# Optimization experiments

Measured on AMD Instinct MI355X. Metric: run time of the kernel, lower is better.

## Reference

```python
import jax, jax.numpy as jnp
import numpy as np

N_TOKEN = 16384
N_EMBED = 512


def setup_inputs() -> dict:
    key = jax.random.key(0)
    k1, k2, k3, k4 = jax.random.split(key, 4)
    inputs = jax.random.normal(k1, (8, 2048, N_EMBED), dtype=jnp.float32)
    # nn.Linear(n_embed, n_token): weight [n_token, n_embed], bias [n_token]
    lin_w = jax.random.normal(k2, (N_TOKEN, N_EMBED), dtype=jnp.float32) * (1.0 / np.sqrt(N_EMBED))
    lin_b = jax.random.normal(k3, (N_TOKEN,), dtype=jnp.float32) * 0.01
    # nn.Embedding(n_token, n_embed) weight = value embeddings
    value_w = jax.random.normal(k4, (N_TOKEN, N_EMBED), dtype=jnp.float32)
    return {"inputs": inputs, "lin_w": lin_w, "lin_b": lin_b, "value_w": value_w}


def reference(inputs, lin_w, lin_b, value_w):
    size = inputs.shape
    x = inputs.reshape(-1, N_EMBED)                       # [T, E]
    logits = jnp.einsum('te,ne->tn', x, lin_w) + lin_b    # [T, N]
    probs = jax.nn.softmax(logits, axis=-1)               # [T, N]
    quantized = jnp.einsum('tn,ne->te', probs, value_w) + x
    return quantized.reshape(size)
```

## Files before the change

### kernel.cpp

```cpp
#include <hip/hip_runtime.h>
#include <hip/hip_bf16.h>
#include <stdint.h>

#define N_TOKEN 16384
#define N_EMBED 512
#define QBLK 64
#define KVB 64
#define NT (N_TOKEN / KVB)

typedef __attribute__((ext_vector_type(8))) short bf16x8;
typedef __attribute__((ext_vector_type(4))) float f32x4;

__device__ __forceinline__ unsigned short f2bf(float f) {
  unsigned u = __float_as_uint(f);
  u = (u + 0x7FFFu + ((u >> 16) & 1u)) >> 16;
  return (unsigned short)u;
}
__device__ __forceinline__ float bf2f(unsigned short h) {
  return __uint_as_float(((unsigned)h) << 16);
}

__device__ __forceinline__ void load_lds16(const void* g, void* l) {
  __builtin_amdgcn_global_load_lds((const __attribute__((address_space(1))) void*)g,
                                   (__attribute__((address_space(3))) void*)l, 16, 0, 0);
}

__global__ void cvt_bf16_kernel(const float* __restrict__ in, unsigned short* __restrict__ out, int n8) {
  int i = blockIdx.x * blockDim.x + threadIdx.x;
  if (i >= n8) return;
  float4 a = ((const float4*)in)[i * 2 + 0];
  float4 b = ((const float4*)in)[i * 2 + 1];
  uint4 o;
  o.x = (unsigned)f2bf(a.x) | ((unsigned)f2bf(a.y) << 16);
  o.y = (unsigned)f2bf(a.z) | ((unsigned)f2bf(a.w) << 16);
  o.z = (unsigned)f2bf(b.x) | ((unsigned)f2bf(b.y) << 16);
  o.w = (unsigned)f2bf(b.z) | ((unsigned)f2bf(b.w) << 16);
  ((uint4*)out)[i] = o;
}

__global__ void transpose_cvt_kernel(const float* __restrict__ in, unsigned short* __restrict__ out) {
  __shared__ float tile[64][65];
  int n0 = blockIdx.x * 64;
  int e0 = blockIdx.y * 64;
  int c = threadIdx.x & 63;
  int r0 = threadIdx.x >> 6;
#pragma unroll
  for (int r = r0; r < 64; r += 4)
    tile[r][c] = in[(size_t)(n0 + r) * N_EMBED + e0 + c];
  __syncthreads();
#pragma unroll
  for (int r = r0; r < 64; r += 4)
    out[(size_t)(e0 + r) * N_TOKEN + n0 + c] = f2bf(tile[c][r]);
}

__global__ __launch_bounds__(512, 2) void flash3_kernel(
    const unsigned short* __restrict__ xb,
    const unsigned short* __restrict__ kb,
    const unsigned short* __restrict__ vt,
    const float* __restrict__ bias,
    const float* __restrict__ xf,
    float* __restrict__ out)
{
  __shared__ __align__(16) unsigned char lds[131072 + 16384 + 8192 + 256];
  unsigned char* Ks = lds;
  unsigned char* Sp = lds + 131072;
  unsigned char* Pb = lds + 131072 + 16384;
  float* lsumB = (float*)(lds + 131072 + 16384 + 8192);

  const int tid = threadIdx.x;
  const int w = tid >> 6;
  const int lane = tid & 63;
  const int g = lane >> 4;
  const int l15 = lane & 15;
  const int wr = w >> 1, we = w & 1;
  const int qbase = blockIdx.x * QBLK;

  if (tid < 64) lsumB[tid] = 0.f;

  bf16x8 q[8];
#pragma unroll
  for (int kk = 0; kk < 8; ++kk)
    q[kk] = *(const bf16x8*)(xb + (size_t)(qbase + 16 * wr + l15) * N_EMBED + 256 * we + 32 * kk + 8 * g);

  const f32x4 fzero = {0.f, 0.f, 0.f, 0.f};
  f32x4 acc[4][4];
#pragma unroll
  for (int rf = 0; rf < 4; ++rf)
#pragma unroll
    for (int cf = 0; cf < 4; ++cf) acc[rf][cf] = fzero;

  auto stage = [&](int half, int t) {
    const unsigned char* kg = (const unsigned char*)(kb + (size_t)t * KVB * N_EMBED);
    unsigned char* Kd = Ks + half * 65536;
#pragma unroll
    for (int it = 0; it < 8; ++it) {
      int c = tid + 512 * it;
      int row = c >> 6;
      int cb = (c & 63) * 16;
      load_lds16(kg + row * 1024 + (cb ^ ((row & 7) << 4)), Kd + c * 16);
    }
  };

  stage(0, 0);

  for (int kt = 0; kt < NT; ++kt) {
    const int buf = kt & 1;
    const unsigned char* Kb = Ks + buf * 65536;

    bf16x8 bv[4][2];
    {
      const unsigned short* vbase = vt + kt * KVB + 8 * g;
#pragma unroll
      for (int cf = 0; cf < 4; ++cf)
#pragma unroll
        for (int ks = 0; ks < 2; ++ks)
          bv[cf][ks] = *(const bf16x8*)(vbase + (size_t)(64 * w + 16 * cf + l15) * N_TOKEN + 32 * ks);
    }

    if (kt + 1 < NT) {
      stage(buf ^ 1, kt + 1);
      asm volatile("s_waitcnt vmcnt(16)" ::: "memory");
    } else {
      asm volatile("s_waitcnt vmcnt(8)" ::: "memory");
    }
    __builtin_amdgcn_sched_barrier(0);
    __builtin_amdgcn_s_barrier();

    f32x4 s[4];
#pragma unroll
    for (int nf = 0; nf < 4; ++nf) s[nf] = fzero;
    __builtin_amdgcn_s_setprio(1);
#pragma unroll
    for (int kk = 0; kk < 8; ++kk) {
      int cb = 512 * we + 64 * kk + 16 * g;
#pragma unroll
      for (int nf = 0; nf < 4; ++nf) {
        int row = 16 * nf + l15;
        bf16x8 bk = *(const bf16x8*)(Kb + row * 1024 + (cb ^ ((row & 7) << 4)));
        s[nf] = __builtin_amdgcn_mfma_f32_16x16x32_bf16(q[kk], bk, s[nf], 0, 0, 0);
      }
    }
    __builtin_amdgcn_s_setprio(0);
#pragma unroll
    for (int nf = 0; nf < 4; ++nf)
#pragma unroll
      for (int j = 0; j < 4; ++j) {
        int row = 16 * wr + 4 * g + j;
        int slot = (2 * nf + (l15 >> 3)) ^ (row & 7);
        *(unsigned short*)(Sp + we * 8192 + row * 128 + 16 * slot + 2 * (l15 & 7)) = f2bf(s[nf][j]);
      }
    asm volatile("s_waitcnt lgkmcnt(0)" ::: "memory");
    __builtin_amdgcn_sched_barrier(0);
    __builtin_amdgcn_s_barrier();

    {
      int row = 8 * w + (lane >> 3);
      int c = lane & 7;
      int off = row * 128 + 16 * (c ^ (row & 7));
      bf16x8 p0 = *(const bf16x8*)(Sp + off);
      bf16x8 p1 = *(const bf16x8*)(Sp + 8192 + off);
      const float* bp = bias + kt * KVB + 8 * c;
      float4 b0 = *(const float4*)bp;
      float4 b1 = *(const float4*)(bp + 4);
      float bb[8] = {b0.x, b0.y, b0.z, b0.w, b1.x, b1.y, b1.z, b1.w};
      bf16x8 pw;
      float ps = 0.f;
#pragma unroll
      for (int i = 0; i < 8; ++i) {
        float v = exp2f((bf2f((unsigned short)p0[i]) + bf2f((unsigned short)p1[i]) + bb[i]) * 1.44269504f);
        pw[i] = (short)f2bf(v);
        ps += v;
      }
      *(bf16x8*)(Pb + off) = pw;
      ps += __shfl_xor(ps, 1, 64);
      ps += __shfl_xor(ps, 2, 64);
      ps += __shfl_xor(ps, 4, 64);
      if (c == 0) lsumB[row] += ps;
    }
    asm volatile("s_waitcnt lgkmcnt(0)" ::: "memory");
    __builtin_amdgcn_sched_barrier(0);
    __builtin_amdgcn_s_barrier();

    __builtin_amdgcn_s_setprio(1);
#pragma unroll
    for (int ks = 0; ks < 2; ++ks) {
      bf16x8 pa[4];
#pragma unroll
      for (int rf = 0; rf < 4; ++rf) {
        int row = 16 * rf + l15;
        pa[rf] = *(const bf16x8*)(Pb + row * 128 + 16 * ((4 * ks + g) ^ (row & 7)));
      }
#pragma unroll
      for (int cf = 0; cf < 4; ++cf)
#pragma unroll
        for (int rf = 0; rf < 4; ++rf)
          acc[rf][cf] = __builtin_amdgcn_mfma_f32_16x16x32_bf16(pa[rf], bv[cf][ks], acc[rf][cf], 0, 0, 0);
    }
    __builtin_amdgcn_s_setprio(0);
  }

#pragma unroll
  for (int rf = 0; rf < 4; ++rf)
#pragma unroll
    for (int j = 0; j < 4; ++j) {
      int lrow = 16 * rf + 4 * g + j;
      float inv = 1.0f / lsumB[lrow];
      int row = qbase + lrow;
#pragma unroll
      for (int cf = 0; cf < 4; ++cf) {
        int col = 64 * w + 16 * cf + l15;
        size_t idx = (size_t)row * N_EMBED + col;
        out[idx] = acc[rf][cf][j] * inv + xf[idx];
      }
    }
}

extern "C" void kernel_launch(void* const* d_in, const int* in_sizes, int n_in,
                              void* d_out, int out_size, void* d_ws, size_t ws_size,
                              hipStream_t stream) {
  const float* x = (const float*)d_in[0];
  const float* lin_w = (const float*)d_in[1];
  const float* lin_b = (const float*)d_in[2];
  const float* value_w = (const float*)d_in[3];
  float* outp = (float*)d_out;

  unsigned short* xb = (unsigned short*)d_ws;
  unsigned short* wb = (unsigned short*)((char*)d_ws + (16 << 20));
  unsigned short* vt = (unsigned short*)((char*)d_ws + (32 << 20));

  const int n8 = (N_TOKEN * N_EMBED) / 8;
  cvt_bf16_kernel<<<n8 / 256, 256, 0, stream>>>(x, xb, n8);
  cvt_bf16_kernel<<<n8 / 256, 256, 0, stream>>>(lin_w, wb, n8);
  transpose_cvt_kernel<<<dim3(N_TOKEN / 64, N_EMBED / 64), 256, 0, stream>>>(value_w, vt);
  flash3_kernel<<<N_TOKEN / QBLK, 512, 0, stream>>>(xb, wb, vt, lin_b, x, outp);
}
```

Measured before the change: 1.216 ms.

## Software-pipeline flash kernel over three stages with smaller key blocks

Halves the key/value block to 32 tokens and reorganises the main loop into a three-stage software pipeline: QK^T for tile t, softmax/exp for tile t-1 and PV accumulation for tile t-2 run in the same iteration, so each step needs one barrier instead of three. Waves are re-split so each computes all 64 query rows over a quarter of the embedding, and partial logits are reduced through double-buffered LDS. Row sums now stay in registers and are reduced once at the end. LDS use drops, but launch bounds go from 2 to 1 block per CU and q fragments take more registers, which may cut occupancy and latency hiding.

```diff
diff --git a/kernel.cpp b/kernel.cpp
--- a/kernel.cpp
+++ b/kernel.cpp
@@ -5,10 +5,11 @@
 #define N_TOKEN 16384
 #define N_EMBED 512
 #define QBLK 64
-#define KVB 64
+#define KVB 32
 #define NT (N_TOKEN / KVB)
 
 typedef __attribute__((ext_vector_type(8))) short bf16x8;
+typedef __attribute__((ext_vector_type(4))) short bf16x4;
 typedef __attribute__((ext_vector_type(4))) float f32x4;
 
 __device__ __forceinline__ unsigned short f2bf(float f) {
@@ -53,7 +54,7 @@
     out[(size_t)(e0 + r) * N_TOKEN + n0 + c] = f2bf(tile[c][r]);
 }
 
-__global__ __launch_bounds__(512, 2) void flash3_kernel(
+__global__ __launch_bounds__(512, 1) void flash4_kernel(
     const unsigned short* __restrict__ xb,
     const unsigned short* __restrict__ kb,
     const unsigned short* __restrict__ vt,
@@ -61,26 +62,27 @@
     const float* __restrict__ xf,
     float* __restrict__ out)
 {
-  __shared__ __align__(16) unsigned char lds[131072 + 16384 + 8192 + 256];
+  __shared__ __align__(16) unsigned char lds[65536 + 36864 + 8192 + 256];
   unsigned char* Ks = lds;
-  unsigned char* Sp = lds + 131072;
-  unsigned char* Pb = lds + 131072 + 16384;
-  float* lsumB = (float*)(lds + 131072 + 16384 + 8192);
+  unsigned char* Sp = lds + 65536;
+  unsigned char* Pb = lds + 65536 + 36864;
+  float* lsumB = (float*)(lds + 65536 + 36864 + 8192);
 
   const int tid = threadIdx.x;
   const int w = tid >> 6;
   const int lane = tid & 63;
   const int g = lane >> 4;
   const int l15 = lane & 15;
-  const int wr = w >> 1, we = w & 1;
+  const int we = w >> 1, wn = w & 1;
   const int qbase = blockIdx.x * QBLK;
 
-  if (tid < 64) lsumB[tid] = 0.f;
-
-  bf16x8 q[8];
-#pragma unroll
-  for (int kk = 0; kk < 8; ++kk)
-    q[kk] = *(const bf16x8*)(xb + (size_t)(qbase + 16 * wr + l15) * N_EMBED + 256 * we + 32 * kk + 8 * g);
+  bf16x8 q[4][4];
+#pragma unroll
+  for (int rf = 0; rf < 4; ++rf)
+#pragma unroll
+    for (int kk = 0; kk < 4; ++kk)
+      q[rf][kk] = *(const bf16x8*)(xb + (size_t)(qbase + 16 * rf + l15) * N_EMBED +
+                                   128 * we + 32 * kk + 8 * g);
 
   const f32x4 fzero = {0.f, 0.f, 0.f, 0.f};
   f32x4 acc[4][4];
@@ -88,12 +90,16 @@
   for (int rf = 0; rf < 4; ++rf)
 #pragma unroll
     for (int cf = 0; cf < 4; ++cf) acc[rf][cf] = fzero;
+  float lsum_reg = 0.f;
+
+  const int eq = 8 * w + (lane >> 3);
+  const int ec = lane & 7;
 
   auto stage = [&](int half, int t) {
     const unsigned char* kg = (const unsigned char*)(kb + (size_t)t * KVB * N_EMBED);
-    unsigned char* Kd = Ks + half * 65536;
-#pragma unroll
-    for (int it = 0; it < 8; ++it) {
+    unsigned char* Kd = Ks + half * 32768;
+#pragma unroll
+    for (int it = 0; it < 4; ++it) {
       int c = tid + 512 * it;
       int row = c >> 6;
       int cb = (c & 63) * 16;
@@ -103,109 +109,106 @@
 
   stage(0, 0);
 
-  for (int kt = 0; kt < NT; ++kt) {
-    const int buf = kt & 1;
-    const unsigned char* Kb = Ks + buf * 65536;
-
-    bf16x8 bv[4][2];
-    {
-      const unsigned short* vbase = vt + kt * KVB + 8 * g;
-#pragma unroll
-      for (int cf = 0; cf < 4; ++cf)
-#pragma unroll
-        for (int ks = 0; ks < 2; ++ks)
-          bv[cf][ks] = *(const bf16x8*)(vbase + (size_t)(64 * w + 16 * cf + l15) * N_TOKEN + 32 * ks);
-    }
-
-    if (kt + 1 < NT) {
-      stage(buf ^ 1, kt + 1);
-      asm volatile("s_waitcnt vmcnt(16)" ::: "memory");
-    } else {
-      asm volatile("s_waitcnt vmcnt(8)" ::: "memory");
-    }
+  for (int t = 0; t < NT + 2; ++t) {
+    asm volatile("s_waitcnt vmcnt(0) lgkmcnt(0)" ::: "memory");
     __builtin_amdgcn_sched_barrier(0);
     __builtin_amdgcn_s_barrier();
 
-    f32x4 s[4];
-#pragma unroll
-    for (int nf = 0; nf < 4; ++nf) s[nf] = fzero;
-    __builtin_amdgcn_s_setprio(1);
-#pragma unroll
-    for (int kk = 0; kk < 8; ++kk) {
-      int cb = 512 * we + 64 * kk + 16 * g;
-#pragma unroll
-      for (int nf = 0; nf < 4; ++nf) {
-        int row = 16 * nf + l15;
-        bf16x8 bk = *(const bf16x8*)(Kb + row * 1024 + (cb ^ ((row & 7) << 4)));
-        s[nf] = __builtin_amdgcn_mfma_f32_16x16x32_bf16(q[kk], bk, s[nf], 0, 0, 0);
+    bf16x8 bv[4];
+    if (t >= 2) {
+      const unsigned short* vbase = vt + (size_t)(t - 2) * KVB + 8 * g;
+#pragma unroll
+      for (int cf = 0; cf < 4; ++cf)
+        bv[cf] = *(const bf16x8*)(vbase + (size_t)(64 * w + 16 * cf + l15) * N_TOKEN);
+    }
+    if (t + 1 < NT) stage((t + 1) & 1, t + 1);
+
+    if (t < NT) {
+      const unsigned char* Kb = Ks + (t & 1) * 32768;
+      f32x4 s[4];
+#pragma unroll
+      for (int rf = 0; rf < 4; ++rf) s[rf] = fzero;
+      const int krow = 16 * wn + l15;
+      __builtin_amdgcn_s_setprio(1);
+#pragma unroll
+      for (int kk = 0; kk < 4; ++kk) {
+        int cb = 256 * we + 64 * kk + 16 * g;
+        bf16x8 bk = *(const bf16x8*)(Kb + krow * 1024 + (cb ^ ((krow & 7) << 4)));
+#pragma unroll
+        for (int rf = 0; rf < 4; ++rf)
+          s[rf] = __builtin_amdgcn_mfma_f32_16x16x32_bf16(q[rf][kk], bk, s[rf], 0, 0, 0);
       }
-    }
-    __builtin_amdgcn_s_setprio(0);
-#pragma unroll
-    for (int nf = 0; nf < 4; ++nf)
-#pragma unroll
-      for (int j = 0; j < 4; ++j) {
-        int row = 16 * wr + 4 * g + j;
-        int slot = (2 * nf + (l15 >> 3)) ^ (row & 7);
-        *(unsigned short*)(Sp + we * 8192 + row * 128 + 16 * slot + 2 * (l15 & 7)) = f2bf(s[nf][j]);
-      }
-    asm volatile("s_waitcnt lgkmcnt(0)" ::: "memory");
-    __builtin_amdgcn_sched_barrier(0);
-    __builtin_amdgcn_s_barrier();
-
-    {
-      int row = 8 * w + (lane >> 3);
-      int c = lane & 7;
-      int off = row * 128 + 16 * (c ^ (row & 7));
-      bf16x8 p0 = *(const bf16x8*)(Sp + off);
-      bf16x8 p1 = *(const bf16x8*)(Sp + 8192 + off);
-      const float* bp = bias + kt * KVB + 8 * c;
-      float4 b0 = *(const float4*)bp;
-      float4 b1 = *(const float4*)(bp + 4);
-      float bb[8] = {b0.x, b0.y, b0.z, b0.w, b1.x, b1.y, b1.z, b1.w};
-      bf16x8 pw;
-      float ps = 0.f;
-#pragma unroll
-      for (int i = 0; i < 8; ++i) {
-        float v = exp2f((bf2f((unsigned short)p0[i]) + bf2f((unsigned short)p1[i]) + bb[i]) * 1.44269504f);
-        pw[i] = (short)f2bf(v);
-        ps += v;
-      }
-      *(bf16x8*)(Pb + off) = pw;
-      ps += __shfl_xor(ps, 1, 64);
-      ps += __shfl_xor(ps, 2, 64);
-      ps += __shfl_xor(ps, 4, 64);
-      if (c == 0) lsumB[row] += ps;
-    }
-    asm volatile("s_waitcnt lgkmcnt(0)" ::: "memory");
-    __builtin_amdgcn_sched_barrier(0);
-    __builtin_amdgcn_s_barrier();
-
-    __builtin_amdgcn_s_setprio(1);
-#pragma unroll
-    for (int ks = 0; ks < 2; ++ks) {
+      __builtin_amdgcn_s_setprio(0);
+      unsigned char* sp = Sp + (t & 1) * 18432 + we * 4608;
+#pragma unroll
+      for (int rf = 0; rf < 4; ++rf)
+#pragma unroll
+        for (int j = 0; j < 4; ++j) {
+          int qq = 16 * rf + 4 * g + j;
+          *(unsigned short*)(sp + qq * 72 + (16 * wn + l15) * 2) = f2bf(s[rf][j]);
+        }
+    }
+
+    if (t >= 1 && t <= NT) {
+      const unsigned char* sp = Sp + ((t - 1) & 1) * 18432;
+      int off = eq * 72 + ec * 8;
+      bf16x4 p0 = *(const bf16x4*)(sp + off);
+      bf16x4 p1 = *(const bf16x4*)(sp + 4608 + off);
+      bf16x4 p2 = *(const bf16x4*)(sp + 9216 + off);
+      bf16x4 p3 = *(const bf16x4*)(sp + 13824 + off);
+      float4 bb = *(const float4*)(bias + (t - 1) * KVB + 4 * ec);
+      float l0 = bf2f((unsigned short)p0[0]) + bf2f((unsigned short)p1[0]) +
+                 bf2f((unsigned short)p2[0]) + bf2f((unsigned short)p3[0]) + bb.x;
+      float l1 = bf2f((unsigned short)p0[1]) + bf2f((unsigned short)p1[1]) +
+                 bf2f((unsigned short)p2[1]) + bf2f((unsigned short)p3[1]) + bb.y;
+      float l2 = bf2f((unsigned short)p0[2]) + bf2f((unsigned short)p1[2]) +
+                 bf2f((unsigned short)p2[2]) + bf2f((unsigned short)p3[2]) + bb.z;
+      float l3 = bf2f((unsigned short)p0[3]) + bf2f((unsigned short)p1[3]) +
+                 bf2f((unsigned short)p2[3]) + bf2f((unsigned short)p3[3]) + bb.w;
+      float e0 = exp2f(l0 * 1.44269504f);
+      float e1 = exp2f(l1 * 1.44269504f);
+      float e2 = exp2f(l2 * 1.44269504f);
+      float e3 = exp2f(l3 * 1.44269504f);
+      lsum_reg += (e0 + e1) + (e2 + e3);
+      bf16x4 pw;
+      pw[0] = (short)f2bf(e0);
+      pw[1] = (short)f2bf(e1);
+      pw[2] = (short)f2bf(e2);
+      pw[3] = (short)f2bf(e3);
+      *(bf16x4*)(Pb + ((t - 1) & 1) * 4096 + eq * 64 + ec * 8) = pw;
+    }
+
+    if (t >= 2) {
+      const unsigned char* pb = Pb + (t & 1) * 4096;
       bf16x8 pa[4];
 #pragma unroll
-      for (int rf = 0; rf < 4; ++rf) {
-        int row = 16 * rf + l15;
-        pa[rf] = *(const bf16x8*)(Pb + row * 128 + 16 * ((4 * ks + g) ^ (row & 7)));
-      }
+      for (int rf = 0; rf < 4; ++rf)
+        pa[rf] = *(const bf16x8*)(pb + (16 * rf + l15) * 64 + g * 16);
+      __builtin_amdgcn_s_setprio(1);
 #pragma unroll
       for (int cf = 0; cf < 4; ++cf)
 #pragma unroll
         for (int rf = 0; rf < 4; ++rf)
-          acc[rf][cf] = __builtin_amdgcn_mfma_f32_16x16x32_bf16(pa[rf], bv[cf][ks], acc[rf][cf], 0, 0, 0);
-    }
-    __builtin_amdgcn_s_setprio(0);
+          acc[rf][cf] = __builtin_amdgcn_mfma_f32_16x16x32_bf16(pa[rf], bv[cf], acc[rf][cf], 0, 0, 0);
+      __builtin_amdgcn_s_setprio(0);
+    }
   }
 
+  {
+    float r = lsum_reg;
+    r += __shfl_xor(r, 1, 64);
+    r += __shfl_xor(r, 2, 64);
+    r += __shfl_xor(r, 4, 64);
+    if (ec == 0) lsumB[eq] = r;
+  }
+  __syncthreads();
 #pragma unroll
   for (int rf = 0; rf < 4; ++rf)
 #pragma unroll
     for (int j = 0; j < 4; ++j) {
-      int lrow = 16 * rf + 4 * g + j;
-      float inv = 1.0f / lsumB[lrow];
-      int row = qbase + lrow;
+      int qq = 16 * rf + 4 * g + j;
+      float inv = 1.0f / lsumB[qq];
+      int row = qbase + qq;
 #pragma unroll
       for (int cf = 0; cf < 4; ++cf) {
         int col = 64 * w + 16 * cf + l15;
@@ -232,5 +235,5 @@
   cvt_bf16_kernel<<<n8 / 256, 256, 0, stream>>>(x, xb, n8);
   cvt_bf16_kernel<<<n8 / 256, 256, 0, stream>>>(lin_w, wb, n8);
   transpose_cvt_kernel<<<dim3(N_TOKEN / 64, N_EMBED / 64), 256, 0, stream>>>(value_w, vt);
-  flash3_kernel<<<N_TOKEN / QBLK, 512, 0, stream>>>(xb, wb, vt, lin_b, x, outp);
-}
+  flash4_kernel<<<N_TOKEN / QBLK, 512, 0, stream>>>(xb, wb, vt, lin_b, x, outp);
+}
```

After: 1.076 ms. 11.5% less time.
